# Performance work log

Measured on AMD Instinct MI355X. Metric: run time of the kernel, lower is better.

Reference implementation:

```python
import jax, jax.numpy as jnp
import numpy as np

BN_EPS = 1e-5
NUM_GRAPHS = 64


def _gin_layer(x, src, dst, eps, w1, b1, gamma, beta, w2, b2):
    # GIN aggregation: sum of source features into destination nodes
    n = x.shape[0]
    agg = jax.ops.segment_sum(x[src], dst, num_segments=n)  # [N, d]
    h = (1.0 + eps) * x + agg
    # MLP: Linear -> BatchNorm1d (batch stats, train mode) -> ReLU -> Linear
    h = h @ w1 + b1
    mu = jnp.mean(h, axis=0)
    var = jnp.var(h, axis=0)
    h = gamma * (h - mu) * jax.lax.rsqrt(var + BN_EPS) + beta
    h = jax.nn.relu(h)
    return h @ w2 + b2


def setup_inputs() -> dict:
    key = jax.random.key(0)
    ks = jax.random.split(key, 16)
    N, E, F = 100000, 3200000, 128
    x = jax.random.normal(ks[0], (N, F), dtype=jnp.float32)
    edge_index = jax.random.randint(ks[1], (2, E), 0, N, dtype=jnp.int64)
    batch = jnp.sort(jax.random.randint(ks[2], (N,), 0, NUM_GRAPHS, dtype=jnp.int64))

    def lin(k, fin, fout):
        kw, kb = jax.random.split(k)
        s = 1.0 / np.sqrt(fin)
        w = jax.random.uniform(kw, (fin, fout), jnp.float32, -s, s)
        b = jax.random.uniform(kb, (fout,), jnp.float32, -s, s)
        return w, b

    w1a, b1a = lin(ks[3], F, 64)
    w1b, b1b = lin(ks[4], 64, 32)
    w2a, b2a = lin(ks[5], 32, 64)
    w2b, b2b = lin(ks[6], 64, 16)
    lw, lb = lin(ks[7], 16, 1)
    return {
        "x": x, "edge_index": edge_index, "batch": batch,
        "eps1": jnp.float32(0.0), "eps2": jnp.float32(0.0),
        "w1a": w1a, "b1a": b1a, "g1": jnp.ones(64, jnp.float32), "bt1": jnp.zeros(64, jnp.float32),
        "w1b": w1b, "b1b": b1b,
        "w2a": w2a, "b2a": b2a, "g2": jnp.ones(64, jnp.float32), "bt2": jnp.zeros(64, jnp.float32),
        "w2b": w2b, "b2b": b2b,
        "lw": lw, "lb": lb,
    }


def reference(x, edge_index, batch, eps1, eps2, w1a, b1a, g1, bt1, w1b, b1b,
              w2a, b2a, g2, bt2, w2b, b2b, lw, lb):
    src, dst = edge_index[0], edge_index[1]
    h = _gin_layer(x, src, dst, eps1, w1a, b1a, g1, bt1, w1b, b1b)   # [N, 32]
    h = _gin_layer(h, src, dst, eps2, w2a, b2a, g2, bt2, w2b, b2b)   # [N, 16]
    # global mean pool over graphs
    sums = jax.ops.segment_sum(h, batch, num_segments=NUM_GRAPHS)    # [G, 16]
    counts = jax.ops.segment_sum(jnp.ones((h.shape[0],), h.dtype), batch,
                                 num_segments=NUM_GRAPHS)
    pooled = sums / jnp.maximum(counts, 1.0)[:, None]
    return jax.nn.sigmoid(pooled @ lw + lb)                           # [G, 1]
```

## Files before the change

kernel.cpp:

```cpp
#include <hip/hip_runtime.h>
#include <hip/hip_fp16.h>
#include <math.h>

#define G_GRAPHS 64
#define BIN_SHIFT 7
#define BIN_SIZE 128
#define NBINS_CAP 1024
#define C_CHUNK 16384

__device__ __forceinline__ void fma4(float4& a, float s, float4 w) {
    a.x += s * w.x; a.y += s * w.y; a.z += s * w.z; a.w += s * w.w;
}
__device__ __forceinline__ float4 h4_to_f4(ushort4 u) {
    return make_float4(__half2float(__ushort_as_half(u.x)),
                       __half2float(__ushort_as_half(u.y)),
                       __half2float(__ushort_as_half(u.z)),
                       __half2float(__ushort_as_half(u.w)));
}
__device__ __forceinline__ ushort4 f4_to_h4(float4 f) {
    ushort4 u;
    u.x = __half_as_ushort(__float2half_rn(f.x));
    u.y = __half_as_ushort(__float2half_rn(f.y));
    u.z = __half_as_ushort(__float2half_rn(f.z));
    u.w = __half_as_ushort(__float2half_rn(f.w));
    return u;
}

__device__ __forceinline__ float4 fp8x4_to_f4(unsigned int w) {
#if __has_builtin(__builtin_amdgcn_cvt_f32_fp8)
    float4 r;
    r.x = __builtin_amdgcn_cvt_f32_fp8((int)w, 0);
    r.y = __builtin_amdgcn_cvt_f32_fp8((int)w, 1);
    r.z = __builtin_amdgcn_cvt_f32_fp8((int)w, 2);
    r.w = __builtin_amdgcn_cvt_f32_fp8((int)w, 3);
    return r;
#else
    const float sc = 1.329227995784916e+36f;
    unsigned b0 = w & 0xffu, b1 = (w >> 8) & 0xffu,
             b2 = (w >> 16) & 0xffu, b3 = (w >> 24) & 0xffu;
    float4 r;
    r.x = __uint_as_float(((b0 & 0x80u) << 24) | ((b0 & 0x7fu) << 20)) * sc;
    r.y = __uint_as_float(((b1 & 0x80u) << 24) | ((b1 & 0x7fu) << 20)) * sc;
    r.z = __uint_as_float(((b2 & 0x80u) << 24) | ((b2 & 0x7fu) << 20)) * sc;
    r.w = __uint_as_float(((b3 & 0x80u) << 24) | ((b3 & 0x7fu) << 20)) * sc;
    return r;
#endif
}
__device__ __forceinline__ unsigned int f4_to_fp8x4(float4 f) {
#if __has_builtin(__builtin_amdgcn_cvt_pk_fp8_f32)
    int v = __builtin_amdgcn_cvt_pk_fp8_f32(f.x, f.y, 0, false);
    v = __builtin_amdgcn_cvt_pk_fp8_f32(f.z, f.w, v, true);
    return (unsigned int)v;
#else
    const float sc = 7.52316384526264e-37f;
    float vv[4] = {f.x, f.y, f.z, f.w};
    unsigned out = 0;
    #pragma unroll
    for (int i = 0; i < 4; ++i) {
        unsigned u = __float_as_uint(vv[i] * sc);
        unsigned s = (u >> 24) & 0x80u;
        u += 0x00080000u;
        unsigned m = (u >> 20) & 0x7fu;
        out |= (s | m) << (8 * i);
    }
    return out;
#endif
}

__global__ __launch_bounds__(256) void k_binA(
    const int* __restrict__ dst, int* __restrict__ binCnt, int nE, int nbins,
    int vec4ok)
{
    __shared__ int cnt[NBINS_CAP];
    for (int i = threadIdx.x; i < nbins; i += 256) cnt[i] = 0;
    __syncthreads();
    int base = blockIdx.x * C_CHUNK;
    int end  = min(base + C_CHUNK, nE);
    int done = base;
    if (vec4ok) {
        int cnt4 = (end - base) >> 2;
        const int4* d4 = (const int4*)(dst + base);
        for (int i = threadIdx.x; i < cnt4; i += 256) {
            int4 v = d4[i];
            atomicAdd(&cnt[v.x >> BIN_SHIFT], 1);
            atomicAdd(&cnt[v.y >> BIN_SHIFT], 1);
            atomicAdd(&cnt[v.z >> BIN_SHIFT], 1);
            atomicAdd(&cnt[v.w >> BIN_SHIFT], 1);
        }
        done = base + (cnt4 << 2);
    }
    for (int e = done + threadIdx.x; e < end; e += 256)
        atomicAdd(&cnt[dst[e] >> BIN_SHIFT], 1);
    __syncthreads();
    for (int i = threadIdx.x; i < nbins; i += 256)
        if (cnt[i]) atomicAdd(&binCnt[i], cnt[i]);
}

__global__ __launch_bounds__(1024) void k_binB(
    const int* __restrict__ binCnt, int nbins, int nE,
    int* __restrict__ binOff, int* __restrict__ binCur,
    int* __restrict__ off, int n)
{
    __shared__ int sb[1024];
    int tid = threadIdx.x;
    int v = (tid < nbins) ? binCnt[tid] : 0;
    sb[tid] = v;
    __syncthreads();
    for (int d = 1; d < 1024; d <<= 1) {
        int t = (tid >= d) ? sb[tid - d] : 0;
        __syncthreads();
        sb[tid] += t;
        __syncthreads();
    }
    if (tid < nbins) {
        int ex = sb[tid] - v;
        binOff[tid] = ex; binCur[tid] = ex;
    }
    if (tid == 0) { binOff[nbins] = nE; off[n] = nE; }
}

__global__ __launch_bounds__(256) void k_binC(
    const int* __restrict__ src, const int* __restrict__ dst,
    int* __restrict__ binCur, int* __restrict__ staging, int nE, int nbins,
    int vec4ok)
{
    __shared__ int cnt[NBINS_CAP];
    for (int i = threadIdx.x; i < nbins; i += 256) cnt[i] = 0;
    __syncthreads();
    int base = blockIdx.x * C_CHUNK;
    int end  = min(base + C_CHUNK, nE);
    int done = base;
    if (vec4ok) {
        int cnt4 = (end - base) >> 2;
        const int4* d4 = (const int4*)(dst + base);
        for (int i = threadIdx.x; i < cnt4; i += 256) {
            int4 v = d4[i];
            atomicAdd(&cnt[v.x >> BIN_SHIFT], 1);
            atomicAdd(&cnt[v.y >> BIN_SHIFT], 1);
            atomicAdd(&cnt[v.z >> BIN_SHIFT], 1);
            atomicAdd(&cnt[v.w >> BIN_SHIFT], 1);
        }
        done = base + (cnt4 << 2);
    }
    for (int e = done + threadIdx.x; e < end; e += 256)
        atomicAdd(&cnt[dst[e] >> BIN_SHIFT], 1);
    __syncthreads();
    for (int i = threadIdx.x; i < nbins; i += 256) {
        int c = cnt[i];
        cnt[i] = c ? atomicAdd(&binCur[i], c) : 0;
    }
    __syncthreads();
    if (vec4ok) {
        int cnt4 = (end - base) >> 2;
        const int4* d4 = (const int4*)(dst + base);
        const int4* s4 = (const int4*)(src + base);
        for (int i = threadIdx.x; i < cnt4; i += 256) {
            int4 dv = d4[i]; int4 sv = s4[i];
            int b, p;
            b = dv.x >> BIN_SHIFT; p = atomicAdd(&cnt[b], 1);
            staging[p] = ((dv.x & (BIN_SIZE-1)) << 17) | sv.x;
            b = dv.y >> BIN_SHIFT; p = atomicAdd(&cnt[b], 1);
            staging[p] = ((dv.y & (BIN_SIZE-1)) << 17) | sv.y;
            b = dv.z >> BIN_SHIFT; p = atomicAdd(&cnt[b], 1);
            staging[p] = ((dv.z & (BIN_SIZE-1)) << 17) | sv.z;
            b = dv.w >> BIN_SHIFT; p = atomicAdd(&cnt[b], 1);
            staging[p] = ((dv.w & (BIN_SIZE-1)) << 17) | sv.w;
        }
    }
    for (int e = done + threadIdx.x; e < end; e += 256) {
        int d = dst[e], s = src[e];
        int b = d >> BIN_SHIFT;
        int p = atomicAdd(&cnt[b], 1);
        staging[p] = ((d & (BIN_SIZE - 1)) << 17) | s;
    }
}

__global__ __launch_bounds__(256) void k_binD(
    const int* __restrict__ binOff, const int* __restrict__ staging,
    int* __restrict__ off, int* __restrict__ csr, int n)
{
    __shared__ int deg[BIN_SIZE];
    __shared__ int cur[BIN_SIZE];
    int b = blockIdx.x;
    int s = binOff[b], e = binOff[b + 1];
    int tid = threadIdx.x;
    if (tid < BIN_SIZE) deg[tid] = 0;
    __syncthreads();
    for (int j = s + tid; j < e; j += 256)
        atomicAdd(&deg[staging[j] >> 17], 1);
    __syncthreads();
    if (tid < BIN_SIZE) cur[tid] = deg[tid];
    __syncthreads();
    for (int d = 1; d < BIN_SIZE; d <<= 1) {
        int t = (tid >= d && tid < BIN_SIZE) ? cur[tid - d] : 0;
        __syncthreads();
        if (tid < BIN_SIZE) cur[tid] += t;
        __syncthreads();
    }
    if (tid < BIN_SIZE) {
        int node = b * BIN_SIZE + tid;
        int ex = s + cur[tid] - deg[tid];
        if (node < n) off[node] = ex;
        cur[tid] = ex;
    }
    __syncthreads();
    for (int j = s + tid; j < e; j += 256) {
        int pk = staging[j];
        int p = atomicAdd(&cur[pk >> 17], 1);
        csr[p] = pk & 0x1FFFF;
    }
}

__global__ __launch_bounds__(256) void k_gemm1(
    const float* __restrict__ x, const float* __restrict__ w1a,
    unsigned int* __restrict__ y8, int n)
{
    __shared__ float  xs[64 * 129];
    __shared__ float4 ws[128 * 16];
    int tid = threadIdx.x;
    const float4* w4 = (const float4*)w1a;
    #pragma unroll
    for (int i = tid; i < 128 * 16; i += 256) ws[i] = w4[i];
    int row0 = blockIdx.x * 64;
    for (int i = tid; i < 64 * 32; i += 256) {
        int r = i >> 5, k4 = i & 31;
        float4 v = {0.f, 0.f, 0.f, 0.f};
        if (row0 + r < n) v = ((const float4*)x)[(size_t)(row0 + r) * 32 + k4];
        xs[r * 129 + k4 * 4 + 0] = v.x;
        xs[r * 129 + k4 * 4 + 1] = v.y;
        xs[r * 129 + k4 * 4 + 2] = v.z;
        xs[r * 129 + k4 * 4 + 3] = v.w;
    }
    __syncthreads();
    int c4 = tid & 15, rg = tid >> 4;
    float4 acc[4] = {{0,0,0,0},{0,0,0,0},{0,0,0,0},{0,0,0,0}};
    const float* xr = xs + rg * 4 * 129;
    #pragma unroll 8
    for (int k = 0; k < 128; ++k) {
        float4 wv = ws[k * 16 + c4];
        fma4(acc[0], xr[k +   0], wv);
        fma4(acc[1], xr[k + 129], wv);
        fma4(acc[2], xr[k + 258], wv);
        fma4(acc[3], xr[k + 387], wv);
    }
    #pragma unroll
    for (int i = 0; i < 4; ++i) {
        int row = row0 + rg * 4 + i;
        if (row < n) y8[(size_t)row * 16 + c4] = f4_to_fp8x4(acc[i]);
    }
}

__global__ __launch_bounds__(256) void k_agg1(
    const unsigned int* __restrict__ y8, const int* __restrict__ off,
    const int* __restrict__ csr, const float* __restrict__ b1a,
    const float* __restrict__ eps1p, __half* __restrict__ h1, int n,
    float* __restrict__ p_sum, float* __restrict__ p_sq)
{
    __shared__ float s_sum[4][64];
    __shared__ float s_sq[4][64];
    int slot = threadIdx.x >> 6;
    int lane = threadIdx.x & 63;
    int node = blockIdx.x * 4 + slot;
    int c = lane & 15;
    int g = lane >> 4;
    bool valid = node < n;
    int o = 0, e = 0;
    if (valid) { o = off[node]; e = off[node + 1]; }
    float4 acc = {0.f, 0.f, 0.f, 0.f};
    float4 acc2 = {0.f, 0.f, 0.f, 0.f};
    if (valid && g == 0) {
        float4 v = fp8x4_to_f4(y8[(size_t)node * 16 + c]);
        float4 bv = ((const float4*)b1a)[c];
        float ep = 1.0f + eps1p[0];
        acc.x = ep * v.x + bv.x; acc.y = ep * v.y + bv.y;
        acc.z = ep * v.z + bv.z; acc.w = ep * v.w + bv.w;
    }
    int j = o + g;
    for (; j + 12 < e; j += 16) {
        int s0 = csr[j], s1 = csr[j + 4], s2 = csr[j + 8], s3 = csr[j + 12];
        unsigned w0 = y8[(size_t)s0 * 16 + c];
        unsigned w1 = y8[(size_t)s1 * 16 + c];
        unsigned w2 = y8[(size_t)s2 * 16 + c];
        unsigned w3 = y8[(size_t)s3 * 16 + c];
        float4 v0 = fp8x4_to_f4(w0);
        float4 v1 = fp8x4_to_f4(w1);
        float4 v2 = fp8x4_to_f4(w2);
        float4 v3 = fp8x4_to_f4(w3);
        acc.x  += v0.x + v1.x; acc.y  += v0.y + v1.y;
        acc.z  += v0.z + v1.z; acc.w  += v0.w + v1.w;
        acc2.x += v2.x + v3.x; acc2.y += v2.y + v3.y;
        acc2.z += v2.z + v3.z; acc2.w += v2.w + v3.w;
    }
    for (; j < e; j += 4) {
        float4 v = fp8x4_to_f4(y8[(size_t)csr[j] * 16 + c]);
        acc.x += v.x; acc.y += v.y; acc.z += v.z; acc.w += v.w;
    }
    acc.x += acc2.x; acc.y += acc2.y; acc.z += acc2.z; acc.w += acc2.w;
    acc.x += __shfl_xor(acc.x, 16, 64); acc.x += __shfl_xor(acc.x, 32, 64);
    acc.y += __shfl_xor(acc.y, 16, 64); acc.y += __shfl_xor(acc.y, 32, 64);
    acc.z += __shfl_xor(acc.z, 16, 64); acc.z += __shfl_xor(acc.z, 32, 64);
    acc.w += __shfl_xor(acc.w, 16, 64); acc.w += __shfl_xor(acc.w, 32, 64);
    if (g == 0) {
        if (valid) ((ushort4*)h1)[(size_t)node * 16 + c] = f4_to_h4(acc);
        float vx = valid ? acc.x : 0.f, vy = valid ? acc.y : 0.f;
        float vz = valid ? acc.z : 0.f, vw = valid ? acc.w : 0.f;
        s_sum[slot][4*c+0] = vx; s_sum[slot][4*c+1] = vy;
        s_sum[slot][4*c+2] = vz; s_sum[slot][4*c+3] = vw;
        s_sq[slot][4*c+0] = vx*vx; s_sq[slot][4*c+1] = vy*vy;
        s_sq[slot][4*c+2] = vz*vz; s_sq[slot][4*c+3] = vw*vw;
    }
    __syncthreads();
    if (threadIdx.x < 64) {
        int col = threadIdx.x;
        float s = s_sum[0][col] + s_sum[1][col] + s_sum[2][col] + s_sum[3][col];
        float q = s_sq[0][col]  + s_sq[1][col]  + s_sq[2][col]  + s_sq[3][col];
        int ps = (blockIdx.x & 63) * 64 + col;
        atomicAdd(&p_sum[ps], s);
        atomicAdd(&p_sq[ps], q);
    }
}

__global__ __launch_bounds__(256) void k_agg2(
    const unsigned int* __restrict__ h28, const int* __restrict__ off,
    const int* __restrict__ csr, const float* __restrict__ eps2p,
    __half* __restrict__ agg2h, int n)
{
    int node = blockIdx.x * 4 + (threadIdx.x >> 6);
    if (node >= n) return;
    int lane = threadIdx.x & 63;
    int c = lane & 7;
    int g = lane >> 3;
    int o = off[node], e = off[node + 1];
    float4 acc = {0.f, 0.f, 0.f, 0.f};
    float4 acc2 = {0.f, 0.f, 0.f, 0.f};
    if (g == 0) {
        float4 v = fp8x4_to_f4(h28[(size_t)node * 8 + c]);
        float ep = 1.0f + eps2p[0];
        acc.x = ep * v.x; acc.y = ep * v.y; acc.z = ep * v.z; acc.w = ep * v.w;
    }
    int j = o + g;
    for (; j + 24 < e; j += 32) {
        int s0 = csr[j], s1 = csr[j + 8], s2 = csr[j + 16], s3 = csr[j + 24];
        unsigned w0 = h28[(size_t)s0 * 8 + c];
        unsigned w1 = h28[(size_t)s1 * 8 + c];
        unsigned w2 = h28[(size_t)s2 * 8 + c];
        unsigned w3 = h28[(size_t)s3 * 8 + c];
        float4 v0 = fp8x4_to_f4(w0);
        float4 v1 = fp8x4_to_f4(w1);
        float4 v2 = fp8x4_to_f4(w2);
        float4 v3 = fp8x4_to_f4(w3);
        acc.x  += v0.x + v1.x; acc.y  += v0.y + v1.y;
        acc.z  += v0.z + v1.z; acc.w  += v0.w + v1.w;
        acc2.x += v2.x + v3.x; acc2.y += v2.y + v3.y;
        acc2.z += v2.z + v3.z; acc2.w += v2.w + v3.w;
    }
    for (; j < e; j += 8) {
        float4 v = fp8x4_to_f4(h28[(size_t)csr[j] * 8 + c]);
        acc.x += v.x; acc.y += v.y; acc.z += v.z; acc.w += v.w;
    }
    acc.x += acc2.x; acc.y += acc2.y; acc.z += acc2.z; acc.w += acc2.w;
    acc.x += __shfl_xor(acc.x, 8, 64); acc.x += __shfl_xor(acc.x, 16, 64); acc.x += __shfl_xor(acc.x, 32, 64);
    acc.y += __shfl_xor(acc.y, 8, 64); acc.y += __shfl_xor(acc.y, 16, 64); acc.y += __shfl_xor(acc.y, 32, 64);
    acc.z += __shfl_xor(acc.z, 8, 64); acc.z += __shfl_xor(acc.z, 16, 64); acc.z += __shfl_xor(acc.z, 32, 64);
    acc.w += __shfl_xor(acc.w, 8, 64); acc.w += __shfl_xor(acc.w, 16, 64); acc.w += __shfl_xor(acc.w, 32, 64);
    if (g == 0)
        ((ushort4*)agg2h)[(size_t)node * 8 + c] = f4_to_h4(acc);
}

__global__ void k_bnfin(const float* __restrict__ p_sum, const float* __restrict__ p_sq,
                        const float* __restrict__ gamma, const float* __restrict__ beta,
                        float nf, float* __restrict__ a, float* __restrict__ c)
{
    int i = threadIdx.x;
    float s = 0.f, q = 0.f;
    for (int k = 0; k < 64; ++k) { s += p_sum[k*64 + i]; q += p_sq[k*64 + i]; }
    float mu  = s / nf;
    float var = q / nf - mu * mu;
    float av  = gamma[i] * rsqrtf(var + 1e-5f);
    a[i] = av;
    c[i] = beta[i] - av * mu;
}

__global__ __launch_bounds__(256) void k_mlp1b(
    const __half* __restrict__ h1, const float* __restrict__ a1,
    const float* __restrict__ c1, const float* __restrict__ w1b,
    const float* __restrict__ b1b, unsigned int* __restrict__ h28, int n)
{
    __shared__ float  xs[128 * 65];
    __shared__ float4 ws[64 * 8];
    __shared__ float  as[64], cs[64];
    int tid = threadIdx.x;
    #pragma unroll
    for (int i = tid; i < 64 * 8; i += 256) ws[i] = ((const float4*)w1b)[i];
    if (tid < 64) { as[tid] = a1[tid]; cs[tid] = c1[tid]; }
    __syncthreads();
    int row0 = blockIdx.x * 128;
    for (int i = tid; i < 128 * 16; i += 256) {
        int r = i >> 4, k4 = i & 15;
        float4 v = {0.f, 0.f, 0.f, 0.f};
        if (row0 + r < n) {
            v = h4_to_f4(((const ushort4*)h1)[(size_t)(row0 + r) * 16 + k4]);
            v.x = fmaxf(as[k4*4+0] * v.x + cs[k4*4+0], 0.f);
            v.y = fmaxf(as[k4*4+1] * v.y + cs[k4*4+1], 0.f);
            v.z = fmaxf(as[k4*4+2] * v.z + cs[k4*4+2], 0.f);
            v.w = fmaxf(as[k4*4+3] * v.w + cs[k4*4+3], 0.f);
        }
        xs[r * 65 + k4 * 4 + 0] = v.x;
        xs[r * 65 + k4 * 4 + 1] = v.y;
        xs[r * 65 + k4 * 4 + 2] = v.z;
        xs[r * 65 + k4 * 4 + 3] = v.w;
    }
    __syncthreads();
    int c4 = tid & 7, rg = tid >> 3;
    float4 bv = ((const float4*)b1b)[c4];
    float4 acc[4] = {bv, bv, bv, bv};
    const float* xr = xs + rg * 4 * 65;
    #pragma unroll 8
    for (int k = 0; k < 64; ++k) {
        float4 wv = ws[k * 8 + c4];
        fma4(acc[0], xr[k +   0], wv);
        fma4(acc[1], xr[k +  65], wv);
        fma4(acc[2], xr[k + 130], wv);
        fma4(acc[3], xr[k + 195], wv);
    }
    #pragma unroll
    for (int i = 0; i < 4; ++i) {
        int row = row0 + rg * 4 + i;
        if (row < n) h28[(size_t)row * 8 + c4] = f4_to_fp8x4(acc[i]);
    }
}

__global__ __launch_bounds__(256) void k_gemm2(
    const __half* __restrict__ agg2h, const float* __restrict__ w2a,
    const float* __restrict__ b2a, __half* __restrict__ h3, int n,
    float* __restrict__ p_sum, float* __restrict__ p_sq)
{
    __shared__ float  xs[64 * 33];
    __shared__ float4 ws[32 * 16];
    __shared__ float  s_sum[64], s_sq[64];
    int tid = threadIdx.x;
    if (tid < 64) { s_sum[tid] = 0.f; s_sq[tid] = 0.f; }
    #pragma unroll
    for (int i = tid; i < 32 * 16; i += 256) ws[i] = ((const float4*)w2a)[i];
    int row0 = blockIdx.x * 64;
    for (int i = tid; i < 64 * 8; i += 256) {
        int r = i >> 3, k4 = i & 7;
        float4 v = {0.f, 0.f, 0.f, 0.f};
        if (row0 + r < n) v = h4_to_f4(((const ushort4*)agg2h)[(size_t)(row0 + r) * 8 + k4]);
        xs[r * 33 + k4 * 4 + 0] = v.x;
        xs[r * 33 + k4 * 4 + 1] = v.y;
        xs[r * 33 + k4 * 4 + 2] = v.z;
        xs[r * 33 + k4 * 4 + 3] = v.w;
    }
    __syncthreads();
    int c4 = tid & 15, rg = tid >> 4;
    float4 bv = ((const float4*)b2a)[c4];
    float4 acc[4] = {bv, bv, bv, bv};
    const float* xr = xs + rg * 4 * 33;
    #pragma unroll
    for (int k = 0; k < 32; ++k) {
        float4 wv = ws[k * 16 + c4];
        fma4(acc[0], xr[k +  0], wv);
        fma4(acc[1], xr[k + 33], wv);
        fma4(acc[2], xr[k + 66], wv);
        fma4(acc[3], xr[k + 99], wv);
    }
    float cs_[4] = {0,0,0,0}, cq_[4] = {0,0,0,0};
    #pragma unroll
    for (int i = 0; i < 4; ++i) {
        int row = row0 + rg * 4 + i;
        if (row < n) {
            ((ushort4*)h3)[(size_t)row * 16 + c4] = f4_to_h4(acc[i]);
            cs_[0] += acc[i].x; cq_[0] += acc[i].x * acc[i].x;
            cs_[1] += acc[i].y; cq_[1] += acc[i].y * acc[i].y;
            cs_[2] += acc[i].z; cq_[2] += acc[i].z * acc[i].z;
            cs_[3] += acc[i].w; cq_[3] += acc[i].w * acc[i].w;
        }
    }
    #pragma unroll
    for (int jj = 0; jj < 4; ++jj) {
        atomicAdd(&s_sum[c4 * 4 + jj], cs_[jj]);
        atomicAdd(&s_sq[c4 * 4 + jj],  cq_[jj]);
    }
    __syncthreads();
    if (tid < 64) {
        int ps = (blockIdx.x & 63) * 64 + tid;
        atomicAdd(&p_sum[ps], s_sum[tid]);
        atomicAdd(&p_sq[ps],  s_sq[tid]);
    }
}

__global__ __launch_bounds__(256) void k_final(
    const __half* __restrict__ h3, const float* __restrict__ a2,
    const float* __restrict__ c2, const float* __restrict__ w2b,
    const float* __restrict__ b2b, const int* __restrict__ batch,
    float* __restrict__ pool, float* __restrict__ cnt, int n)
{
    __shared__ float  xs[64 * 65];
    __shared__ float4 ws[64 * 4];
    __shared__ float  as[64], cs[64];
    __shared__ float  pl[G_GRAPHS * 16];
    __shared__ float  cl[G_GRAPHS];
    int tid = threadIdx.x;
    for (int i = tid; i < 256; i += 256) ws[i] = ((const float4*)w2b)[i];
    if (tid < 64) { as[tid] = a2[tid]; cs[tid] = c2[tid]; cl[tid] = 0.f; }
    for (int i = tid; i < G_GRAPHS * 16; i += 256) pl[i] = 0.f;
    __syncthreads();
    int row0 = blockIdx.x * 64;
    for (int i = tid; i < 64 * 16; i += 256) {
        int r = i >> 4, k4 = i & 15;
        float4 v = {0.f, 0.f, 0.f, 0.f};
        if (row0 + r < n) {
            v = h4_to_f4(((const ushort4*)h3)[(size_t)(row0 + r) * 16 + k4]);
            v.x = fmaxf(as[k4*4+0] * v.x + cs[k4*4+0], 0.f);
            v.y = fmaxf(as[k4*4+1] * v.y + cs[k4*4+1], 0.f);
            v.z = fmaxf(as[k4*4+2] * v.z + cs[k4*4+2], 0.f);
            v.w = fmaxf(as[k4*4+3] * v.w + cs[k4*4+3], 0.f);
        }
        xs[r * 65 + k4 * 4 + 0] = v.x;
        xs[r * 65 + k4 * 4 + 1] = v.y;
        xs[r * 65 + k4 * 4 + 2] = v.z;
        xs[r * 65 + k4 * 4 + 3] = v.w;
    }
    __syncthreads();
    int c4 = tid & 3, r = tid >> 2;
    float4 acc = ((const float4*)b2b)[c4];
    const float* xr = xs + r * 65;
    #pragma unroll 8
    for (int k = 0; k < 64; ++k) {
        float4 wv = ws[k * 4 + c4];
        fma4(acc, xr[k], wv);
    }
    int row = row0 + r;
    if (row < n) {
        int g = batch[row];
        if (c4 == 0) atomicAdd(&cl[g], 1.f);
        float* pp = &pl[g * 16 + c4 * 4];
        atomicAdd(pp + 0, acc.x); atomicAdd(pp + 1, acc.y);
        atomicAdd(pp + 2, acc.z); atomicAdd(pp + 3, acc.w);
    }
    __syncthreads();
    if (tid < 64 && cl[tid] != 0.f) atomicAdd(&cnt[tid], cl[tid]);
    for (int i = tid; i < G_GRAPHS * 16; i += 256) {
        int g = i >> 4;
        if (cl[g] != 0.f) atomicAdd(&pool[i], pl[i]);
    }
}

__global__ void k_head(const float* __restrict__ pool, const float* __restrict__ cnt,
                       const float* __restrict__ lw, const float* __restrict__ lb,
                       float* __restrict__ out)
{
    int g = threadIdx.x;
    float cv = fmaxf(cnt[g], 1.0f);
    float acc = lb[0];
    #pragma unroll
    for (int f = 0; f < 16; ++f) acc += (pool[g * 16 + f] / cv) * lw[f];
    out[g] = 1.0f / (1.0f + expf(-acc));
}

extern "C" void kernel_launch(void* const* d_in, const int* in_sizes, int n_in,
                              void* d_out, int out_size, void* d_ws, size_t ws_size,
                              hipStream_t stream)
{
    const float* x    = (const float*)d_in[0];
    const int*   eidx = (const int*)d_in[1];
    const int*   batch= (const int*)d_in[2];
    const float* eps1 = (const float*)d_in[3];
    const float* eps2 = (const float*)d_in[4];
    const float* w1a  = (const float*)d_in[5];
    const float* b1a  = (const float*)d_in[6];
    const float* g1   = (const float*)d_in[7];
    const float* bt1  = (const float*)d_in[8];
    const float* w1b  = (const float*)d_in[9];
    const float* b1b  = (const float*)d_in[10];
    const float* w2a  = (const float*)d_in[11];
    const float* b2a  = (const float*)d_in[12];
    const float* g2   = (const float*)d_in[13];
    const float* bt2  = (const float*)d_in[14];
    const float* w2b  = (const float*)d_in[15];
    const float* b2b  = (const float*)d_in[16];
    const float* lw   = (const float*)d_in[17];
    const float* lb   = (const float*)d_in[18];
    float* out = (float*)d_out;

    int n  = in_sizes[0] / 128;
    int nE = in_sizes[1] / 2;
    const int* srcI = eidx;
    const int* dstI = eidx + nE;
    int vec4ok = ((nE & 3) == 0) && ((((uintptr_t)eidx) & 15) == 0);

    char* wsb = (char*)d_ws;
    size_t nn = (size_t)n;
    unsigned int* y8  = (unsigned int*)wsb;
    __half* h1        = (__half*)(wsb + nn * 64);
    unsigned int* h28 = (unsigned int*)(wsb + nn * 192);
    __half* agg2h     = (__half*)(wsb + nn * 224);
    __half* h3        = h1;
    float* stats = (float*)(wsb + nn * 288);
    float* a1     = stats;          float* c1     = stats + 64;
    float* a2     = stats + 128;    float* c2     = stats + 192;
    float* pool   = stats + 256;    float* cntb   = stats + 1280;
    float* p_sum1 = stats + 1344;   float* p_sq1  = stats + 5440;
    float* p_sum2 = stats + 9536;   float* p_sq2  = stats + 13632;

    int* off     = (int*)(stats + 17728);
    int* csr     = off + (n + 1);
    int* binCnt  = csr + nE;
    int* binOff  = binCnt + NBINS_CAP + 1;
    int* binCur  = binOff + NBINS_CAP + 1;
    int* staging = binCur + NBINS_CAP + 1;

    int nbins = (n + BIN_SIZE - 1) >> BIN_SHIFT;

    hipMemsetAsync(stats + 256, 0, (17728 - 256) * sizeof(float), stream);
    hipMemsetAsync(binCnt, 0, (size_t)nbins * sizeof(int), stream);

    int tiles64  = (n + 63) / 64;
    int tiles128 = (n + 127) / 128;
    int cblocks  = (nE + C_CHUNK - 1) / C_CHUNK;
    int nblocks4 = (n + 3) / 4;

    k_gemm1<<<tiles64, 256, 0, stream>>>(x, w1a, y8, n);

    k_binA<<<cblocks, 256, 0, stream>>>(dstI, binCnt, nE, nbins, vec4ok);
    k_binB<<<1, 1024, 0, stream>>>(binCnt, nbins, nE, binOff, binCur, off, n);
    k_binC<<<cblocks, 256, 0, stream>>>(srcI, dstI, binCur, staging, nE, nbins, vec4ok);
    k_binD<<<nbins, 256, 0, stream>>>(binOff, staging, off, csr, n);

    k_agg1<<<nblocks4, 256, 0, stream>>>(y8, off, csr, b1a, eps1, h1, n, p_sum1, p_sq1);
    k_bnfin<<<1, 64, 0, stream>>>(p_sum1, p_sq1, g1, bt1, (float)n, a1, c1);
    k_mlp1b<<<tiles128, 256, 0, stream>>>(h1, a1, c1, w1b, b1b, h28, n);
    k_agg2<<<nblocks4, 256, 0, stream>>>(h28, off, csr, eps2, agg2h, n);
    k_gemm2<<<tiles64, 256, 0, stream>>>(agg2h, w2a, b2a, h3, n, p_sum2, p_sq2);
    k_bnfin<<<1, 64, 0, stream>>>(p_sum2, p_sq2, g2, bt2, (float)n, a2, c2);
    k_final<<<tiles64, 256, 0, stream>>>(h3, a2, c2, w2b, b2b, batch, pool, cntb, n);
    k_head<<<1, 64, 0, stream>>>(pool, cntb, lw, lb, out);
}
```

Measured before the change: 311.1 us.

## Split layer-1 gather into two column-half passes for cache locality

The GEMM1 output is now written as two separate fp8 arrays, each holding 32 columns (32 bytes per node), instead of one 64-byte-per-node array. The layer-1 aggregation runs twice, once per half, with 8 lanes per column group and 8 edge groups per wavefront. Each pass touches a feature table half the size, which should fit better in L2/MALL and cut random-gather misses. The cost is reading the CSR indices twice and an extra launch, plus each gathered row is now a 32-byte access.

```diff
diff --git a/kernel.cpp b/kernel.cpp
--- a/kernel.cpp
+++ b/kernel.cpp
@@ -213,7 +213,7 @@
 
 __global__ __launch_bounds__(256) void k_gemm1(
     const float* __restrict__ x, const float* __restrict__ w1a,
-    unsigned int* __restrict__ y8, int n)
+    unsigned int* __restrict__ ya8, unsigned int* __restrict__ yb8, int n)
 {
     __shared__ float  xs[64 * 129];
     __shared__ float4 ws[128 * 16];
@@ -243,45 +243,47 @@
         fma4(acc[2], xr[k + 258], wv);
         fma4(acc[3], xr[k + 387], wv);
     }
+    unsigned int* tb = (c4 < 8) ? ya8 : yb8;
+    int cc = c4 & 7;
     #pragma unroll
     for (int i = 0; i < 4; ++i) {
         int row = row0 + rg * 4 + i;
-        if (row < n) y8[(size_t)row * 16 + c4] = f4_to_fp8x4(acc[i]);
-    }
-}
-
-__global__ __launch_bounds__(256) void k_agg1(
-    const unsigned int* __restrict__ y8, const int* __restrict__ off,
+        if (row < n) tb[(size_t)row * 8 + cc] = f4_to_fp8x4(acc[i]);
+    }
+}
+
+__global__ __launch_bounds__(256) void k_agg1h(
+    const unsigned int* __restrict__ yh, const int* __restrict__ off,
     const int* __restrict__ csr, const float* __restrict__ b1a,
-    const float* __restrict__ eps1p, __half* __restrict__ h1, int n,
+    const float* __restrict__ eps1p, __half* __restrict__ h1, int n, int colBase,
     float* __restrict__ p_sum, float* __restrict__ p_sq)
 {
-    __shared__ float s_sum[4][64];
-    __shared__ float s_sq[4][64];
+    __shared__ float s_sum[4][32];
+    __shared__ float s_sq[4][32];
     int slot = threadIdx.x >> 6;
     int lane = threadIdx.x & 63;
     int node = blockIdx.x * 4 + slot;
-    int c = lane & 15;
-    int g = lane >> 4;
+    int c = lane & 7;
+    int g = lane >> 3;
     bool valid = node < n;
     int o = 0, e = 0;
     if (valid) { o = off[node]; e = off[node + 1]; }
     float4 acc = {0.f, 0.f, 0.f, 0.f};
     float4 acc2 = {0.f, 0.f, 0.f, 0.f};
     if (valid && g == 0) {
-        float4 v = fp8x4_to_f4(y8[(size_t)node * 16 + c]);
-        float4 bv = ((const float4*)b1a)[c];
+        float4 v = fp8x4_to_f4(yh[(size_t)node * 8 + c]);
+        float4 bv = ((const float4*)(b1a + colBase))[c];
         float ep = 1.0f + eps1p[0];
         acc.x = ep * v.x + bv.x; acc.y = ep * v.y + bv.y;
         acc.z = ep * v.z + bv.z; acc.w = ep * v.w + bv.w;
     }
     int j = o + g;
-    for (; j + 12 < e; j += 16) {
-        int s0 = csr[j], s1 = csr[j + 4], s2 = csr[j + 8], s3 = csr[j + 12];
-        unsigned w0 = y8[(size_t)s0 * 16 + c];
-        unsigned w1 = y8[(size_t)s1 * 16 + c];
-        unsigned w2 = y8[(size_t)s2 * 16 + c];
-        unsigned w3 = y8[(size_t)s3 * 16 + c];
+    for (; j + 24 < e; j += 32) {
+        int s0 = csr[j], s1 = csr[j + 8], s2 = csr[j + 16], s3 = csr[j + 24];
+        unsigned w0 = yh[(size_t)s0 * 8 + c];
+        unsigned w1 = yh[(size_t)s1 * 8 + c];
+        unsigned w2 = yh[(size_t)s2 * 8 + c];
+        unsigned w3 = yh[(size_t)s3 * 8 + c];
         float4 v0 = fp8x4_to_f4(w0);
         float4 v1 = fp8x4_to_f4(w1);
         float4 v2 = fp8x4_to_f4(w2);
@@ -291,17 +293,17 @@
         acc2.x += v2.x + v3.x; acc2.y += v2.y + v3.y;
         acc2.z += v2.z + v3.z; acc2.w += v2.w + v3.w;
     }
-    for (; j < e; j += 4) {
-        float4 v = fp8x4_to_f4(y8[(size_t)csr[j] * 16 + c]);
+    for (; j < e; j += 8) {
+        float4 v = fp8x4_to_f4(yh[(size_t)csr[j] * 8 + c]);
         acc.x += v.x; acc.y += v.y; acc.z += v.z; acc.w += v.w;
     }
     acc.x += acc2.x; acc.y += acc2.y; acc.z += acc2.z; acc.w += acc2.w;
-    acc.x += __shfl_xor(acc.x, 16, 64); acc.x += __shfl_xor(acc.x, 32, 64);
-    acc.y += __shfl_xor(acc.y, 16, 64); acc.y += __shfl_xor(acc.y, 32, 64);
-    acc.z += __shfl_xor(acc.z, 16, 64); acc.z += __shfl_xor(acc.z, 32, 64);
-    acc.w += __shfl_xor(acc.w, 16, 64); acc.w += __shfl_xor(acc.w, 32, 64);
+    acc.x += __shfl_xor(acc.x, 8, 64); acc.x += __shfl_xor(acc.x, 16, 64); acc.x += __shfl_xor(acc.x, 32, 64);
+    acc.y += __shfl_xor(acc.y, 8, 64); acc.y += __shfl_xor(acc.y, 16, 64); acc.y += __shfl_xor(acc.y, 32, 64);
+    acc.z += __shfl_xor(acc.z, 8, 64); acc.z += __shfl_xor(acc.z, 16, 64); acc.z += __shfl_xor(acc.z, 32, 64);
+    acc.w += __shfl_xor(acc.w, 8, 64); acc.w += __shfl_xor(acc.w, 16, 64); acc.w += __shfl_xor(acc.w, 32, 64);
     if (g == 0) {
-        if (valid) ((ushort4*)h1)[(size_t)node * 16 + c] = f4_to_h4(acc);
+        if (valid) ((ushort4*)h1)[(size_t)node * 16 + (colBase >> 2) + c] = f4_to_h4(acc);
         float vx = valid ? acc.x : 0.f, vy = valid ? acc.y : 0.f;
         float vz = valid ? acc.z : 0.f, vw = valid ? acc.w : 0.f;
         s_sum[slot][4*c+0] = vx; s_sum[slot][4*c+1] = vy;
@@ -310,11 +312,11 @@
         s_sq[slot][4*c+2] = vz*vz; s_sq[slot][4*c+3] = vw*vw;
     }
     __syncthreads();
-    if (threadIdx.x < 64) {
+    if (threadIdx.x < 32) {
         int col = threadIdx.x;
         float s = s_sum[0][col] + s_sum[1][col] + s_sum[2][col] + s_sum[3][col];
         float q = s_sq[0][col]  + s_sq[1][col]  + s_sq[2][col]  + s_sq[3][col];
-        int ps = (blockIdx.x & 63) * 64 + col;
+        int ps = (blockIdx.x & 63) * 64 + colBase + col;
         atomicAdd(&p_sum[ps], s);
         atomicAdd(&p_sq[ps], q);
     }
@@ -592,7 +594,8 @@
 
     char* wsb = (char*)d_ws;
     size_t nn = (size_t)n;
-    unsigned int* y8  = (unsigned int*)wsb;
+    unsigned int* ya8 = (unsigned int*)wsb;
+    unsigned int* yb8 = (unsigned int*)(wsb + nn * 32);
     __half* h1        = (__half*)(wsb + nn * 64);
     unsigned int* h28 = (unsigned int*)(wsb + nn * 192);
     __half* agg2h     = (__half*)(wsb + nn * 224);
@@ -621,14 +624,15 @@
     int cblocks  = (nE + C_CHUNK - 1) / C_CHUNK;
     int nblocks4 = (n + 3) / 4;
 
-    k_gemm1<<<tiles64, 256, 0, stream>>>(x, w1a, y8, n);
+    k_gemm1<<<tiles64, 256, 0, stream>>>(x, w1a, ya8, yb8, n);
 
     k_binA<<<cblocks, 256, 0, stream>>>(dstI, binCnt, nE, nbins, vec4ok);
     k_binB<<<1, 1024, 0, stream>>>(binCnt, nbins, nE, binOff, binCur, off, n);
     k_binC<<<cblocks, 256, 0, stream>>>(srcI, dstI, binCur, staging, nE, nbins, vec4ok);
     k_binD<<<nbins, 256, 0, stream>>>(binOff, staging, off, csr, n);
 
-    k_agg1<<<nblocks4, 256, 0, stream>>>(y8, off, csr, b1a, eps1, h1, n, p_sum1, p_sq1);
+    k_agg1h<<<nblocks4, 256, 0, stream>>>(ya8, off, csr, b1a, eps1, h1, n, 0,  p_sum1, p_sq1);
+    k_agg1h<<<nblocks4, 256, 0, stream>>>(yb8, off, csr, b1a, eps1, h1, n, 32, p_sum1, p_sq1);
     k_bnfin<<<1, 64, 0, stream>>>(p_sum1, p_sq1, g1, bt1, (float)n, a1, c1);
     k_mlp1b<<<tiles128, 256, 0, stream>>>(h1, a1, c1, w1b, b1b, h28, n);
     k_agg2<<<nblocks4, 256, 0, stream>>>(h28, off, csr, eps2, agg2h, n);
```

Measured after the change: 341.4 us. 1.1x slower.

## Replace recount-in-scatter with per-block bin histogram and column prefix scan

Applied to the files above, without the earlier changes.

The binning pass now stores each chunk's per-bin counts into a global histogram matrix instead of atomically adding them to global bin counts. A new per-bin kernel scans that matrix across chunks, so the scatter kernel starts from exact per-block offsets. This removes the second counting pass over dst and the global atomics on bin cursors in the scatter kernel. In exchange it adds one kernel launch and a histogram of roughly cblocks by nbins ints in the workspace. The column scan assumes there are at most 256 chunks.

```diff
diff --git a/kernel.cpp b/kernel.cpp
--- a/kernel.cpp
+++ b/kernel.cpp
@@ -68,7 +68,7 @@
 }
 
 __global__ __launch_bounds__(256) void k_binA(
-    const int* __restrict__ dst, int* __restrict__ binCnt, int nE, int nbins,
+    const int* __restrict__ dst, int* __restrict__ hist, int nE, int nbins,
     int vec4ok)
 {
     __shared__ int cnt[NBINS_CAP];
@@ -92,14 +92,32 @@
     for (int e = done + threadIdx.x; e < end; e += 256)
         atomicAdd(&cnt[dst[e] >> BIN_SHIFT], 1);
     __syncthreads();
-    for (int i = threadIdx.x; i < nbins; i += 256)
-        if (cnt[i]) atomicAdd(&binCnt[i], cnt[i]);
-}
-
-__global__ __launch_bounds__(1024) void k_binB(
+    int* hrow = hist + (size_t)blockIdx.x * nbins;
+    for (int i = threadIdx.x; i < nbins; i += 256) hrow[i] = cnt[i];
+}
+
+__global__ __launch_bounds__(256) void k_binB1(
+    int* __restrict__ hist, int cblocks, int nbins, int* __restrict__ binCnt)
+{
+    __shared__ int sb[256];
+    int b = blockIdx.x;
+    int t = threadIdx.x;
+    int v = (t < cblocks) ? hist[(size_t)t * nbins + b] : 0;
+    sb[t] = v;
+    __syncthreads();
+    for (int d = 1; d < 256; d <<= 1) {
+        int tt = (t >= d) ? sb[t - d] : 0;
+        __syncthreads();
+        sb[t] += tt;
+        __syncthreads();
+    }
+    if (t < cblocks) hist[(size_t)t * nbins + b] = sb[t] - v;
+    if (t == 0) binCnt[b] = sb[255];
+}
+
+__global__ __launch_bounds__(1024) void k_binB2(
     const int* __restrict__ binCnt, int nbins, int nE,
-    int* __restrict__ binOff, int* __restrict__ binCur,
-    int* __restrict__ off, int n)
+    int* __restrict__ binOff, int* __restrict__ off, int n)
 {
     __shared__ int sb[1024];
     int tid = threadIdx.x;
@@ -112,44 +130,23 @@
         sb[tid] += t;
         __syncthreads();
     }
-    if (tid < nbins) {
-        int ex = sb[tid] - v;
-        binOff[tid] = ex; binCur[tid] = ex;
-    }
+    if (tid < nbins) binOff[tid] = sb[tid] - v;
     if (tid == 0) { binOff[nbins] = nE; off[n] = nE; }
 }
 
-__global__ __launch_bounds__(256) void k_binC(
+__global__ __launch_bounds__(256) void k_binC2(
     const int* __restrict__ src, const int* __restrict__ dst,
-    int* __restrict__ binCur, int* __restrict__ staging, int nE, int nbins,
-    int vec4ok)
+    const int* __restrict__ binOff, const int* __restrict__ hist,
+    int* __restrict__ staging, int nE, int nbins, int vec4ok)
 {
     __shared__ int cnt[NBINS_CAP];
-    for (int i = threadIdx.x; i < nbins; i += 256) cnt[i] = 0;
+    const int* hrow = hist + (size_t)blockIdx.x * nbins;
+    for (int i = threadIdx.x; i < nbins; i += 256)
+        cnt[i] = binOff[i] + hrow[i];
     __syncthreads();
     int base = blockIdx.x * C_CHUNK;
     int end  = min(base + C_CHUNK, nE);
     int done = base;
-    if (vec4ok) {
-        int cnt4 = (end - base) >> 2;
-        const int4* d4 = (const int4*)(dst + base);
-        for (int i = threadIdx.x; i < cnt4; i += 256) {
-            int4 v = d4[i];
-            atomicAdd(&cnt[v.x >> BIN_SHIFT], 1);
-            atomicAdd(&cnt[v.y >> BIN_SHIFT], 1);
-            atomicAdd(&cnt[v.z >> BIN_SHIFT], 1);
-            atomicAdd(&cnt[v.w >> BIN_SHIFT], 1);
-        }
-        done = base + (cnt4 << 2);
-    }
-    for (int e = done + threadIdx.x; e < end; e += 256)
-        atomicAdd(&cnt[dst[e] >> BIN_SHIFT], 1);
-    __syncthreads();
-    for (int i = threadIdx.x; i < nbins; i += 256) {
-        int c = cnt[i];
-        cnt[i] = c ? atomicAdd(&binCur[i], c) : 0;
-    }
-    __syncthreads();
     if (vec4ok) {
         int cnt4 = (end - base) >> 2;
         const int4* d4 = (const int4*)(dst + base);
@@ -166,6 +163,7 @@
             b = dv.w >> BIN_SHIFT; p = atomicAdd(&cnt[b], 1);
             staging[p] = ((dv.w & (BIN_SIZE-1)) << 17) | sv.w;
         }
+        done = base + (cnt4 << 2);
     }
     for (int e = done + threadIdx.x; e < end; e += 256) {
         int d = dst[e], s = src[e];
@@ -604,28 +602,28 @@
     float* p_sum1 = stats + 1344;   float* p_sq1  = stats + 5440;
     float* p_sum2 = stats + 9536;   float* p_sq2  = stats + 13632;
 
+    int cblocks = (nE + C_CHUNK - 1) / C_CHUNK;
+    int nbins   = (n + BIN_SIZE - 1) >> BIN_SHIFT;
+
     int* off     = (int*)(stats + 17728);
     int* csr     = off + (n + 1);
     int* binCnt  = csr + nE;
     int* binOff  = binCnt + NBINS_CAP + 1;
-    int* binCur  = binOff + NBINS_CAP + 1;
-    int* staging = binCur + NBINS_CAP + 1;
-
-    int nbins = (n + BIN_SIZE - 1) >> BIN_SHIFT;
+    int* staging = binOff + NBINS_CAP + 1;
+    int* hist    = staging + nE;
 
     hipMemsetAsync(stats + 256, 0, (17728 - 256) * sizeof(float), stream);
-    hipMemsetAsync(binCnt, 0, (size_t)nbins * sizeof(int), stream);
 
     int tiles64  = (n + 63) / 64;
     int tiles128 = (n + 127) / 128;
-    int cblocks  = (nE + C_CHUNK - 1) / C_CHUNK;
     int nblocks4 = (n + 3) / 4;
 
     k_gemm1<<<tiles64, 256, 0, stream>>>(x, w1a, y8, n);
 
-    k_binA<<<cblocks, 256, 0, stream>>>(dstI, binCnt, nE, nbins, vec4ok);
-    k_binB<<<1, 1024, 0, stream>>>(binCnt, nbins, nE, binOff, binCur, off, n);
-    k_binC<<<cblocks, 256, 0, stream>>>(srcI, dstI, binCur, staging, nE, nbins, vec4ok);
+    k_binA<<<cblocks, 256, 0, stream>>>(dstI, hist, nE, nbins, vec4ok);
+    k_binB1<<<nbins, 256, 0, stream>>>(hist, cblocks, nbins, binCnt);
+    k_binB2<<<1, 1024, 0, stream>>>(binCnt, nbins, nE, binOff, off, n);
+    k_binC2<<<cblocks, 256, 0, stream>>>(srcI, dstI, binOff, hist, staging, nE, nbins, vec4ok);
     k_binD<<<nbins, 256, 0, stream>>>(binOff, staging, off, csr, n);
 
     k_agg1<<<nblocks4, 256, 0, stream>>>(y8, off, csr, b1a, eps1, h1, n, p_sum1, p_sq1);
```

After: 297.6 us. 1.05x faster.
